# Kernel tuning notes

Hardware: AMD Instinct MI355X
Metric: run time of the kernel (lower is better)

## Reference

```python
import jax, jax.numpy as jnp
import numpy as np

N = 100000
E = 3200000
F_IN, F_HID, F_OUT = 256, 16, 40


def setup_inputs() -> dict:
    key = jax.random.key(0)
    ks = jax.random.split(key, 6)
    x = jax.random.normal(ks[0], (N, F_IN), dtype=jnp.float32)
    edge_index = jax.random.randint(ks[1], (2, E), 0, N, dtype=jnp.int64)
    edge_weight = jax.random.uniform(ks[2], (E,), dtype=jnp.float32)
    W1 = jax.random.normal(ks[3], (F_IN, F_HID), dtype=jnp.float32) * (1.0 / np.sqrt(F_IN))
    b1 = jnp.zeros((F_HID,), dtype=jnp.float32)
    W2 = jax.random.normal(ks[4], (F_HID, F_OUT), dtype=jnp.float32) * (1.0 / np.sqrt(F_HID))
    b2 = jnp.zeros((F_OUT,), dtype=jnp.float32)
    return {"x": x, "edge_index": edge_index, "edge_weight": edge_weight,
            "W1": W1, "b1": b1, "W2": W2, "b2": b2}


def _gcn_norm(edge_index, edge_weight, num_nodes):
    # add self-loops with weight 1 (PyG gcn_norm default fill_value=1.0)
    loop = jnp.arange(num_nodes, dtype=edge_index.dtype)
    row = jnp.concatenate([edge_index[0], loop])
    col = jnp.concatenate([edge_index[1], loop])
    w = jnp.concatenate([edge_weight, jnp.ones((num_nodes,), edge_weight.dtype)])
    deg = jax.ops.segment_sum(w, col, num_segments=num_nodes)
    dinv = jnp.where(deg > 0, jax.lax.rsqrt(deg), 0.0)
    norm = dinv[row] * w * dinv[col]  # D^-1/2 A D^-1/2 edge values
    return row, col, norm


def _gcn_conv(x, W, b, row, col, norm, num_nodes):
    h = x @ W                              # transform first (in >= out)
    msg = h[row] * norm[:, None]           # gather + scale  [E+N, out]
    out = jax.ops.segment_sum(msg, col, num_segments=num_nodes)  # scatter-add
    return out + b


def reference(x, edge_index, edge_weight, W1, b1, W2, b2):
    num_nodes = x.shape[0]
    row, col, norm = _gcn_norm(edge_index, edge_weight, num_nodes)
    h = jax.nn.relu(_gcn_conv(x, W1, b1, row, col, norm, num_nodes))
    # F.dropout(training=self.training) is identity in eval mode
    h = _gcn_conv(h, W2, b2, row, col, norm, num_nodes)
    return jax.nn.log_softmax(h, axis=1)
```

## Files before the change

### kernel.cpp

```cpp
#include <hip/hip_runtime.h>
#include <math.h>

#define BS   128
#define BSL  7
#define NBLK 1024

typedef unsigned int uint;

__global__ __launch_bounds__(256) void k_bcount(const int* __restrict__ col,
                                                uint* __restrict__ cnt,
                                                int E, int NB, int chunk) {
    __shared__ uint bins[1024];
    for (int i = threadIdx.x; i < NB; i += 256) bins[i] = 0u;
    __syncthreads();
    int e0 = blockIdx.x * chunk, e1 = min(E, e0 + chunk);
    for (int e = e0 + threadIdx.x * 4; e < e1; e += 1024) {
        int4 c4;
        if (e + 3 < e1) c4 = *(const int4*)(col + e);
        else {
            c4.x = col[e];
            c4.y = (e + 1 < e1) ? col[e + 1] : -1;
            c4.z = (e + 2 < e1) ? col[e + 2] : -1;
            c4.w = (e + 3 < e1) ? col[e + 3] : -1;
        }
        if (c4.x >= 0) atomicAdd(&bins[c4.x >> BSL], 1u);
        if (c4.y >= 0) atomicAdd(&bins[c4.y >> BSL], 1u);
        if (c4.z >= 0) atomicAdd(&bins[c4.z >> BSL], 1u);
        if (c4.w >= 0) atomicAdd(&bins[c4.w >> BSL], 1u);
    }
    __syncthreads();
    for (int i = threadIdx.x; i < NB; i += 256)
        cnt[(size_t)i * NBLK + blockIdx.x] = bins[i];
}

__global__ __launch_bounds__(256) void k_bprefix(uint* __restrict__ cnt,
                                                 uint* __restrict__ tot) {
    __shared__ uint s[256];
    uint* q = cnt + (size_t)blockIdx.x * NBLK;
    int t = threadIdx.x;
    uint v0 = q[t * 4], v1 = q[t * 4 + 1], v2 = q[t * 4 + 2], v3 = q[t * 4 + 3];
    uint s4 = v0 + v1 + v2 + v3;
    s[t] = s4;
    __syncthreads();
    for (int off = 1; off < 256; off <<= 1) {
        uint x = (t >= off) ? s[t - off] : 0u;
        __syncthreads();
        s[t] += x;
        __syncthreads();
    }
    uint excl = s[t] - s4;
    q[t * 4] = excl; q[t * 4 + 1] = excl + v0;
    q[t * 4 + 2] = excl + v0 + v1; q[t * 4 + 3] = excl + v0 + v1 + v2;
    if (t == 255) tot[blockIdx.x] = s[255];
}

__global__ __launch_bounds__(256) void k_scanT(const uint* __restrict__ tot,
                                               uint* __restrict__ bbase, int NB) {
    __shared__ uint s[256];
    __shared__ uint carry;
    int t = threadIdx.x;
    if (t == 0) carry = 0;
    __syncthreads();
    for (int base = 0; base < NB; base += 256) {
        int i = base + t;
        uint v = (i < NB) ? tot[i] : 0u;
        s[t] = v;
        __syncthreads();
        for (int off = 1; off < 256; off <<= 1) {
            uint x = (t >= off) ? s[t - off] : 0u;
            __syncthreads();
            s[t] += x;
            __syncthreads();
        }
        uint c = carry;
        if (i < NB) bbase[i] = c + s[t] - v;
        __syncthreads();
        if (t == 255) carry = c + s[255];
        __syncthreads();
    }
    if (t == 0) bbase[NB] = carry;
}

__global__ __launch_bounds__(256) void k_bscatter(const int* __restrict__ row,
        const int* __restrict__ col, const float* __restrict__ w,
        const uint* __restrict__ cnt, const uint* __restrict__ bbase,
        int2* __restrict__ bsorted, int E, int NB, int chunk) {
    __shared__ uint cur[1024];
    for (int i = threadIdx.x; i < NB; i += 256)
        cur[i] = bbase[i] + cnt[(size_t)i * NBLK + blockIdx.x];
    __syncthreads();
    int e0 = blockIdx.x * chunk, e1 = min(E, e0 + chunk);
    for (int e = e0 + threadIdx.x * 4; e < e1; e += 1024) {
        int4 c4, r4;
        float4 w4;
        if (e + 3 < e1) {
            c4 = *(const int4*)(col + e);
            r4 = *(const int4*)(row + e);
            w4 = *(const float4*)(w + e);
        } else {
            c4.x = col[e]; r4.x = row[e]; w4.x = w[e];
            c4.y = (e + 1 < e1) ? col[e + 1] : -1; r4.y = (e + 1 < e1) ? row[e + 1] : 0;
            w4.y = (e + 1 < e1) ? w[e + 1] : 0.f;
            c4.z = (e + 2 < e1) ? col[e + 2] : -1; r4.z = (e + 2 < e1) ? row[e + 2] : 0;
            w4.z = (e + 2 < e1) ? w[e + 2] : 0.f;
            c4.w = -1; r4.w = 0; w4.w = 0.f;
        }
        int cc[4] = {c4.x, c4.y, c4.z, c4.w};
        int rr[4] = {r4.x, r4.y, r4.z, r4.w};
        float ww[4] = {w4.x, w4.y, w4.z, w4.w};
#pragma unroll
        for (int k = 0; k < 4; k++) {
            if (cc[k] >= 0) {
                uint slot = atomicAdd(&cur[cc[k] >> BSL], 1u);
                bsorted[slot] = make_int2((rr[k] << BSL) | (cc[k] & (BS - 1)),
                                          __float_as_int(ww[k]));
            }
        }
    }
}

__global__ __launch_bounds__(256) void k_fsort(const int2* __restrict__ bsorted,
        const uint* __restrict__ bbase, int2* __restrict__ fsorted,
        uint* __restrict__ nodeoff, float* __restrict__ dv, int N) {
    __shared__ uint hist[BS];
    __shared__ float wa[BS];
    __shared__ uint cur[BS];
    int b = blockIdx.x, t = threadIdx.x;
    if (t < BS) { hist[t] = 0u; wa[t] = 0.f; }
    __syncthreads();
    uint s0 = bbase[b], s1 = bbase[b + 1];
    for (uint k = s0 + t; k < s1; k += 256) {
        int2 v = bsorted[k];
        int lo = v.x & (BS - 1);
        atomicAdd(&hist[lo], 1u);
        atomicAdd(&wa[lo], __int_as_float(v.y));
    }
    __syncthreads();
    uint vv = (t < BS) ? hist[t] : 0u;
    for (int off = 1; off < BS; off <<= 1) {
        uint x = (t < BS && t >= off) ? hist[t - off] : 0u;
        __syncthreads();
        if (t < BS) hist[t] += x;
        __syncthreads();
    }
    if (t < BS) {
        uint base = s0 + (hist[t] - vv);
        cur[t] = base;
        nodeoff[(b << BSL) + t] = base;
        int n = (b << BSL) + t;
        if (n < N) dv[n] = rsqrtf(1.f + wa[t]);
    }
    __syncthreads();
    for (uint k = s0 + t; k < s1; k += 256) {
        int2 v = bsorted[k];
        int lo = v.x & (BS - 1);
        uint slot = atomicAdd(&cur[lo], 1u);
        fsorted[slot] = make_int2(((uint)v.x) >> BSL, v.y);
    }
}

__global__ __launch_bounds__(256) void k_xw1(const float* __restrict__ x,
                                             const float* __restrict__ W1,
                                             float* __restrict__ h, int N) {
    __shared__ float wsh[256 * 16];
    int t = threadIdx.x;
    const float4* w4 = (const float4*)W1;
    float4* wsh4 = (float4*)wsh;
#pragma unroll
    for (int i = 0; i < 4; i++) wsh4[t + i * 256] = w4[t + i * 256];

    int lane = t & 63, kq = t >> 6;
    int r = blockIdx.x * 64 + lane;
    float acc[16];
#pragma unroll
    for (int j = 0; j < 16; j++) acc[j] = 0.f;
    __syncthreads();

    if (r < N) {
        const float4* xr = (const float4*)(x + (size_t)r * 256 + kq * 64);
#pragma unroll 4
        for (int k4 = 0; k4 < 16; k4++) {
            float4 xv = xr[k4];
            int kb = (kq * 64 + k4 * 4) * 16;
#pragma unroll
            for (int kk = 0; kk < 4; kk++) {
                float xs = (&xv.x)[kk];
                const float4* wrow = (const float4*)&wsh[kb + kk * 16];
#pragma unroll
                for (int jq = 0; jq < 4; jq++) {
                    float4 wv = wrow[jq];
                    acc[jq * 4 + 0] = fmaf(xs, wv.x, acc[jq * 4 + 0]);
                    acc[jq * 4 + 1] = fmaf(xs, wv.y, acc[jq * 4 + 1]);
                    acc[jq * 4 + 2] = fmaf(xs, wv.z, acc[jq * 4 + 2]);
                    acc[jq * 4 + 3] = fmaf(xs, wv.w, acc[jq * 4 + 3]);
                }
            }
        }
    }
    __syncthreads();
    if (kq) {
#pragma unroll
        for (int j = 0; j < 16; j++) wsh[((kq - 1) * 64 + lane) * 17 + j] = acc[j];
    }
    __syncthreads();
    if (kq == 0 && r < N) {
#pragma unroll
        for (int j = 0; j < 16; j++)
            acc[j] += wsh[lane * 17 + j] + wsh[(64 + lane) * 17 + j]
                    + wsh[(128 + lane) * 17 + j];
        float4* ho = (float4*)(h + (size_t)r * 16);
#pragma unroll
        for (int jq = 0; jq < 4; jq++)
            ho[jq] = make_float4(acc[jq * 4], acc[jq * 4 + 1],
                                 acc[jq * 4 + 2], acc[jq * 4 + 3]);
    }
}

__global__ __launch_bounds__(256) void k_gather_l1(const int2* __restrict__ sorted,
        const uint* __restrict__ no, const float* __restrict__ dv,
        const float* __restrict__ h, const float* __restrict__ b1,
        float* __restrict__ ho, int N) {
    int wave = threadIdx.x >> 6;
    int node = blockIdx.x * 4 + wave;
    if (node >= N) return;
    int lane = threadIdx.x & 63;
    int slot = lane >> 3, fl = lane & 7;
    uint s0 = no[node], s1 = no[node + 1];
    float dvn = dv[node];
    float2 acc = make_float2(0.f, 0.f);
    uint k = s0 + slot;
    int2 pr = (k < s1) ? sorted[k] : make_int2(0, 0);
    int nit = (int)((s1 - s0 + 7) >> 3);
    for (int it = 0; it < nit; ++it) {
        uint kn = k + 8;
        int2 prn = (kn < s1) ? sorted[kn] : make_int2(0, 0);
        float nr = dv[pr.x] * __int_as_float(pr.y) * dvn;
        float2 hv = *(const float2*)(h + (size_t)pr.x * 16 + fl * 2);
        acc.x = fmaf(nr, hv.x, acc.x);
        acc.y = fmaf(nr, hv.y, acc.y);
        pr = prn; k = kn;
    }
#pragma unroll
    for (int off = 8; off < 64; off <<= 1) {
        acc.x += __shfl_xor(acc.x, off);
        acc.y += __shfl_xor(acc.y, off);
    }
    if (slot == 0) {
        float2 hs = *(const float2*)(h + (size_t)node * 16 + fl * 2);
        float2 bb = *(const float2*)(b1 + fl * 2);
        float2 r;
        r.x = fmaxf(acc.x + dvn * dvn * hs.x + bb.x, 0.f);
        r.y = fmaxf(acc.y + dvn * dvn * hs.y + bb.y, 0.f);
        *(float2*)(ho + (size_t)node * 16 + fl * 2) = r;
    }
}

__global__ __launch_bounds__(256) void k_gather_l2out(const int2* __restrict__ sorted,
        const uint* __restrict__ no, const float* __restrict__ dv,
        const float* __restrict__ h, const float* __restrict__ W2,
        const float* __restrict__ b2, float* __restrict__ out, int N) {
    int wave = threadIdx.x >> 6;
    int node = blockIdx.x * 4 + wave;
    if (node >= N) return;
    int lane = threadIdx.x & 63;
    int slot = lane >> 3, fl = lane & 7;
    uint s0 = no[node], s1 = no[node + 1];
    float dvn = dv[node];
    float2 acc = make_float2(0.f, 0.f);
    uint k = s0 + slot;
    int2 pr = (k < s1) ? sorted[k] : make_int2(0, 0);
    int nit = (int)((s1 - s0 + 7) >> 3);
    for (int it = 0; it < nit; ++it) {
        uint kn = k + 8;
        int2 prn = (kn < s1) ? sorted[kn] : make_int2(0, 0);
        float nr = dv[pr.x] * __int_as_float(pr.y) * dvn;
        float2 hv = *(const float2*)(h + (size_t)pr.x * 16 + fl * 2);
        acc.x = fmaf(nr, hv.x, acc.x);
        acc.y = fmaf(nr, hv.y, acc.y);
        pr = prn; k = kn;
    }
#pragma unroll
    for (int off = 8; off < 64; off <<= 1) {
        acc.x += __shfl_xor(acc.x, off);
        acc.y += __shfl_xor(acc.y, off);
    }
    if (slot == 0) {
        float2 hs = *(const float2*)(h + (size_t)node * 16 + fl * 2);
        acc.x += dvn * dvn * hs.x;
        acc.y += dvn * dvn * hs.y;
    }
    float aj[16];
#pragma unroll
    for (int q = 0; q < 8; q++) {
        aj[2 * q]     = __shfl(acc.x, q);
        aj[2 * q + 1] = __shfl(acc.y, q);
    }
    float logit = -INFINITY;
    if (lane < 40) {
        logit = b2[lane];
#pragma unroll
        for (int q = 0; q < 16; q++) logit += aj[q] * W2[q * 40 + lane];
    }
    float m = logit;
#pragma unroll
    for (int off = 32; off; off >>= 1) m = fmaxf(m, __shfl_xor(m, off));
    float ex = (lane < 40) ? expf(logit - m) : 0.f;
    float ssum = ex;
#pragma unroll
    for (int off = 32; off; off >>= 1) ssum += __shfl_xor(ssum, off);
    if (lane < 40) out[(size_t)node * 40 + lane] = logit - m - logf(ssum);
}

extern "C" void kernel_launch(void* const* d_in, const int* in_sizes, int n_in,
                              void* d_out, int out_size, void* d_ws, size_t ws_size,
                              hipStream_t stream) {
    const float* x  = (const float*)d_in[0];
    const int*   ei = (const int*)d_in[1];
    const float* ew = (const float*)d_in[2];
    const float* W1 = (const float*)d_in[3];
    const float* b1 = (const float*)d_in[4];
    const float* W2 = (const float*)d_in[5];
    const float* b2 = (const float*)d_in[6];
    float* out = (float*)d_out;

    int N = in_sizes[0] / 256;
    int E = in_sizes[2];
    const int* row = ei;
    const int* col = ei + E;

    int NB = (N + BS - 1) >> BSL;
    int chunk = (((E + NBLK - 1) / NBLK) + 3) & ~3;

    uint* ws32 = (uint*)d_ws;
    int2* fsorted = (int2*)ws32;
    int2* bsorted = (int2*)(ws32 + 2 * (size_t)E);
    uint* cnt     = ws32 + 4 * (size_t)E;
    uint* tot     = cnt + (size_t)NB * NBLK;
    uint* bbase   = tot + NB;
    uint* nodeoff = bbase + NB + 1;
    float* dv     = (float*)(nodeoff + (size_t)NB * BS + 1);
    float* h      = (float*)bsorted;
    float* h1     = h + (size_t)N * 16;

    k_bcount  <<<NBLK, 256, 0, stream>>>(col, cnt, E, NB, chunk);
    k_bprefix <<<NB, 256, 0, stream>>>(cnt, tot);
    k_scanT   <<<1, 256, 0, stream>>>(tot, bbase, NB);
    k_bscatter<<<NBLK, 256, 0, stream>>>(row, col, ew, cnt, bbase, bsorted, E, NB, chunk);
    k_fsort   <<<NB, 256, 0, stream>>>(bsorted, bbase, fsorted, nodeoff, dv, N);
    k_xw1     <<<(N + 63) / 64, 256, 0, stream>>>(x, W1, h, N);
    k_gather_l1   <<<(N + 3) / 4, 256, 0, stream>>>(fsorted, nodeoff, dv, h, b1, h1, N);
    k_gather_l2out<<<(N + 3) / 4, 256, 0, stream>>>(fsorted, nodeoff, dv, h1, W2, b2, out, N);
}
```

Baseline: 472.3 us.

## Split x rows across 4 lanes with interleaved K and shuffle reduction in XW1

The x@W1 kernel now assigns 4 adjacent lanes to each row, and each lane reads interleaved float4 chunks. Neighbouring lanes therefore read contiguous memory, which coalesces the x loads instead of having each lane stride across a 1 KB row. Partial sums are combined with wave shuffles instead of a shared-memory reduction and two block barriers. W1 is stored in shared memory with a padded row stride of 28 to reduce bank conflicts from the different K rows each lane reads, at the cost of more LDS per block.

```diff
diff --git a/kernel.cpp b/kernel.cpp
--- a/kernel.cpp
+++ b/kernel.cpp
@@ -159,55 +159,50 @@
     }
 }
 
+#define WST 28
 __global__ __launch_bounds__(256) void k_xw1(const float* __restrict__ x,
                                              const float* __restrict__ W1,
                                              float* __restrict__ h, int N) {
-    __shared__ float wsh[256 * 16];
+    __shared__ float wsh[256 * WST];
     int t = threadIdx.x;
-    const float4* w4 = (const float4*)W1;
-    float4* wsh4 = (float4*)wsh;
-#pragma unroll
-    for (int i = 0; i < 4; i++) wsh4[t + i * 256] = w4[t + i * 256];
-
-    int lane = t & 63, kq = t >> 6;
-    int r = blockIdx.x * 64 + lane;
+    for (int i = t; i < 4096; i += 256)
+        wsh[(i >> 4) * WST + (i & 15)] = W1[i];
+    __syncthreads();
+
+    int lane = t & 63, wv = t >> 6;
+    int q = lane & 3;
+    int r = blockIdx.x * 64 + wv * 16 + (lane >> 2);
     float acc[16];
 #pragma unroll
     for (int j = 0; j < 16; j++) acc[j] = 0.f;
-    __syncthreads();
 
     if (r < N) {
-        const float4* xr = (const float4*)(x + (size_t)r * 256 + kq * 64);
+        const float4* xr = (const float4*)(x + (size_t)r * 256);
 #pragma unroll 4
         for (int k4 = 0; k4 < 16; k4++) {
-            float4 xv = xr[k4];
-            int kb = (kq * 64 + k4 * 4) * 16;
+            float4 xv = xr[q + k4 * 4];
+            int kbase = (q + 4 * k4) * 4;
 #pragma unroll
             for (int kk = 0; kk < 4; kk++) {
                 float xs = (&xv.x)[kk];
-                const float4* wrow = (const float4*)&wsh[kb + kk * 16];
+                const float* wr = &wsh[(kbase + kk) * WST];
 #pragma unroll
                 for (int jq = 0; jq < 4; jq++) {
-                    float4 wv = wrow[jq];
-                    acc[jq * 4 + 0] = fmaf(xs, wv.x, acc[jq * 4 + 0]);
-                    acc[jq * 4 + 1] = fmaf(xs, wv.y, acc[jq * 4 + 1]);
-                    acc[jq * 4 + 2] = fmaf(xs, wv.z, acc[jq * 4 + 2]);
-                    acc[jq * 4 + 3] = fmaf(xs, wv.w, acc[jq * 4 + 3]);
+                    float4 wv4 = *(const float4*)(wr + jq * 4);
+                    acc[jq * 4 + 0] = fmaf(xs, wv4.x, acc[jq * 4 + 0]);
+                    acc[jq * 4 + 1] = fmaf(xs, wv4.y, acc[jq * 4 + 1]);
+                    acc[jq * 4 + 2] = fmaf(xs, wv4.z, acc[jq * 4 + 2]);
+                    acc[jq * 4 + 3] = fmaf(xs, wv4.w, acc[jq * 4 + 3]);
                 }
             }
         }
     }
-    __syncthreads();
-    if (kq) {
-#pragma unroll
-        for (int j = 0; j < 16; j++) wsh[((kq - 1) * 64 + lane) * 17 + j] = acc[j];
-    }
-    __syncthreads();
-    if (kq == 0 && r < N) {
-#pragma unroll
-        for (int j = 0; j < 16; j++)
-            acc[j] += wsh[lane * 17 + j] + wsh[(64 + lane) * 17 + j]
-                    + wsh[(128 + lane) * 17 + j];
+#pragma unroll
+    for (int j = 0; j < 16; j++) {
+        acc[j] += __shfl_xor(acc[j], 1);
+        acc[j] += __shfl_xor(acc[j], 2);
+    }
+    if (q == 0 && r < N) {
         float4* ho = (float4*)(h + (size_t)r * 16);
 #pragma unroll
         for (int jq = 0; jq < 4; jq++)
```

New measurement: 418.2 us. 1.13x faster.
